# Optimization experiments

Measured on AMD Instinct MI355X. Metric: run time of the kernel, lower is better.

Reference implementation:

```python
import jax, jax.numpy as jnp
import numpy as np

B, L, T = 2048, 512, 32


def setup_inputs() -> dict:
    key = jax.random.key(0)
    k1, k2, k3, k4 = jax.random.split(key, 4)
    emit_score = jax.random.normal(k1, (B, L, T), dtype=jnp.float32)
    transition = jax.random.normal(k2, (T, T), dtype=jnp.float32)
    tags = jax.random.randint(k3, (B, L), 0, T, dtype=jnp.int32)
    lengths = jax.random.randint(k4, (B,), 1, L + 1, dtype=jnp.int32)
    return {"emit_score": emit_score, "transition": transition,
            "tags": tags, "lengths": lengths}


def reference(emit_score, transition, tags, lengths):
    # CRF negative log-likelihood (calculate_loss), per-example loss [B].
    b, l, t = emit_score.shape
    mask = jnp.arange(l)[None, :] < lengths[:, None]          # [B,L] bool
    maskf = mask.astype(emit_score.dtype)

    # --- gold path score ---
    gold = jnp.take_along_axis(emit_score, tags[:, :, None], axis=2)[..., 0]  # [B,L]
    trans_gold = transition[tags[:, :-1], tags[:, 1:]]        # [B,L-1]
    gold = gold.at[:, 1:].add(trans_gold)
    total_score = (gold * maskf).sum(axis=1)                  # [B]

    # --- forward algorithm (log partition) via scan over time ---
    emit_tbT = jnp.transpose(emit_score, (1, 0, 2))           # [L,B,T]
    mask_tb = mask.T                                          # [L,B]

    def step(d, x):
        e_t, m_t = x                                          # [B,T], [B]
        # scores[b, prev, next] = d[b,prev] + transition[prev,next] + e_t[b,next]
        scores = d[:, :, None] + transition[None, :, :] + e_t[:, None, :]
        new_d = jax.nn.logsumexp(scores, axis=1)              # [B,T]
        d = jnp.where(m_t[:, None], new_d, d)                 # freeze finished rows
        return d, None

    d0 = emit_tbT[0]                                          # [B,T]
    d, _ = jax.lax.scan(step, d0, (emit_tbT[1:], mask_tb[1:]))
    log_z = jax.nn.logsumexp(d, axis=1)                       # [B]

    return log_z - total_score                                # loss = -llk
```

## Files before the change

kernel.cpp:

```cpp
#include <hip/hip_runtime.h>


constexpr int TT = 32;
constexpr int LL = 512;

#define L2E  1.4426950408889634f
#define LN2f 0.6931471805599453f

template<int I>
__device__ __forceinline__ float bcastf(float v) {
  return __int_as_float(__builtin_amdgcn_ds_swizzle(__float_as_int(v), (I << 5)));
}
template<int X>
__device__ __forceinline__ float swzxf(float v) {
  return __int_as_float(__builtin_amdgcn_ds_swizzle(__float_as_int(v), (X << 10) | 0x1F));
}
__device__ __forceinline__ float bpermf(int byteaddr, float v) {
  return __int_as_float(__builtin_amdgcn_ds_bpermute(byteaddr, __float_as_int(v)));
}

#define MV4(i0) do { \
    float av0 = bcastf<(i0)>(a);     float av1 = bcastf<(i0)+1>(a); \
    float av2 = bcastf<(i0)+2>(a);   float av3 = bcastf<(i0)+3>(a); \
    acc0 = fmaf(av0, Ec[(i0)],   acc0); acc1 = fmaf(av1, Ec[(i0)+1], acc1); \
    acc2 = fmaf(av2, Ec[(i0)+2], acc2); acc3 = fmaf(av3, Ec[(i0)+3], acc3); \
  } while (0)

__global__ __launch_bounds__(256, 1) void crf_fwd(
    const float* __restrict__ emit, const float* __restrict__ trans,
    const int* __restrict__ tags, const int* __restrict__ lengths,
    float* __restrict__ out, int B)
{
  __shared__ float s_trans[TT * TT];
  {
    const float4* t4 = (const float4*)trans;
    ((float4*)s_trans)[threadIdx.x] = t4[threadIdx.x];
  }
  __syncthreads();

  const int lane = threadIdx.x & 31;
  const int b = blockIdx.x * (blockDim.x >> 5) + (threadIdx.x >> 5);
  if (b >= B) return;
  const int gbase4 = (threadIdx.x & 32) << 2;

  float Ec[TT];
#pragma unroll
  for (int i = 0; i < TT; ++i)
    Ec[i] = __builtin_amdgcn_exp2f(s_trans[i * TT + lane] * L2E);

  const int len = lengths[b];
  const float* erow = emit + (size_t)b * (LL * TT);
  const int*  trow = tags + (size_t)b * LL;

  float e0  = erow[lane];
  int  ptag = trow[0];
  float g   = bpermf((ptag << 2) + gbase4, e0);
  float a   = __builtin_amdgcn_exp2f(e0 * L2E);
  float LS  = 0.f;

  int mlen = max(len, __shfl_xor(len, 32));
  mlen = __builtin_amdgcn_readfirstlane(mlen);
  const int nch = (mlen - 1 + 3) >> 2;

  float eb[4], en[4];
  int   tg[4], tgn[4];
#pragma unroll
  for (int k = 0; k < 4; ++k) {
    int t = 1 + k; int tc = t < LL ? t : LL - 1;
    eb[k] = erow[tc * TT + lane];
    tg[k] = trow[tc];
  }
#pragma unroll
  for (int k = 0; k < 4; ++k) {
    int t = 5 + k; int tc = t < LL ? t : LL - 1;
    en[k] = erow[tc * TT + lane];
    tgn[k] = trow[tc];
  }

  for (int c = 0; c < nch; ++c) {
    const int tb = 1 + (c << 2);

    float ep[4]; int tgp[4];
#pragma unroll
    for (int k = 0; k < 4; ++k) {
      int t = tb + 8 + k; int tc = t < LL ? t : LL - 1;
      ep[k]  = erow[tc * TT + lane];
      tgp[k] = trow[tc];
    }

    float e2v[4];
#pragma unroll
    for (int k = 0; k < 4; ++k) e2v[k] = __builtin_amdgcn_exp2f(eb[k] * L2E);

#pragma unroll
    for (int k = 0; k < 4; ++k) {
      const int t = tb + k;
      float acc0 = 0.f, acc1 = 0.f, acc2 = 0.f, acc3 = 0.f;
      MV4(0); MV4(4); MV4(8); MV4(12); MV4(16); MV4(20); MV4(24); MV4(28);
      float anew = ((acc0 + acc1) + (acc2 + acc3)) * e2v[k];
      const bool valid = t < len;
      a = valid ? anew : a;

      int tag  = tg[k];
      float eg = bpermf((tag << 2) + gbase4, eb[k]);
      float tr = s_trans[(ptag << 5) + tag];
      g += valid ? (eg + tr) : 0.f;
      ptag = tag;
    }

    float m = fmaxf(bcastf<0>(a), 1e-30f);
    float r = __builtin_amdgcn_rcpf(m);
    a *= r;
    LS += __builtin_amdgcn_logf(m);

#pragma unroll
    for (int k = 0; k < 4; ++k) {
      eb[k] = en[k]; tg[k] = tgn[k];
      en[k] = ep[k]; tgn[k] = tgp[k];
    }
  }

  float s = a;
  s += swzxf<1>(s); s += swzxf<2>(s); s += swzxf<4>(s);
  s += swzxf<8>(s); s += swzxf<16>(s);
  float logz = (__builtin_amdgcn_logf(s) + LS) * LN2f;
  if (lane == 0) out[b] = logz - g;
}

extern "C" void kernel_launch(void* const* d_in, const int* in_sizes, int n_in,
                              void* d_out, int out_size, void* d_ws, size_t ws_size,
                              hipStream_t stream) {
  const float* emit    = (const float*)d_in[0];
  const float* trans   = (const float*)d_in[1];
  const int*   tags    = (const int*)d_in[2];
  const int*   lengths = (const int*)d_in[3];
  float*       out     = (float*)d_out;
  const int B = in_sizes[3];
  const int groupsPerBlock = 256 / 32;
  const int blocks = (B + groupsPerBlock - 1) / groupsPerBlock;
  hipLaunchKernelGGL(crf_fwd, dim3(blocks), dim3(256), 0, stream,
                     emit, trans, tags, lengths, out, B);
}
```

Measured before the change: 283.1 us.

## Broadcast alpha through LDS float4 reads and shrink blocks to one wave

Replaces the 32 ds_swizzle broadcasts per step with a store of alpha to shared memory followed by eight float4 LDS reads. Blocks go from 256 threads to 64 (one wave, two sequences), giving 1024 blocks instead of 256 so more of the GPU's compute units get work. The gold-score gather via ds_bpermute becomes a per-lane masked accumulation, reduced by swizzle at the end. This adds an LDS write-read round trip on every time step, with no explicit barrier; it relies on the two sequences sharing one wavefront so the 32-lane groups run in lockstep.

```diff
diff --git a/kernel.cpp b/kernel.cpp
--- a/kernel.cpp
+++ b/kernel.cpp
@@ -15,33 +15,29 @@
 __device__ __forceinline__ float swzxf(float v) {
   return __int_as_float(__builtin_amdgcn_ds_swizzle(__float_as_int(v), (X << 10) | 0x1F));
 }
-__device__ __forceinline__ float bpermf(int byteaddr, float v) {
-  return __int_as_float(__builtin_amdgcn_ds_bpermute(byteaddr, __float_as_int(v)));
-}
 
-#define MV4(i0) do { \
-    float av0 = bcastf<(i0)>(a);     float av1 = bcastf<(i0)+1>(a); \
-    float av2 = bcastf<(i0)+2>(a);   float av3 = bcastf<(i0)+3>(a); \
-    acc0 = fmaf(av0, Ec[(i0)],   acc0); acc1 = fmaf(av1, Ec[(i0)+1], acc1); \
-    acc2 = fmaf(av2, Ec[(i0)+2], acc2); acc3 = fmaf(av3, Ec[(i0)+3], acc3); \
-  } while (0)
-
-__global__ __launch_bounds__(256, 1) void crf_fwd(
+__global__ __launch_bounds__(64) void crf_fwd(
     const float* __restrict__ emit, const float* __restrict__ trans,
     const int* __restrict__ tags, const int* __restrict__ lengths,
     float* __restrict__ out, int B)
 {
-  __shared__ float s_trans[TT * TT];
+  __shared__ float  s_trans[TT * TT];
+  __shared__ float4 s_alpha[2][TT / 4];
+
   {
     const float4* t4 = (const float4*)trans;
-    ((float4*)s_trans)[threadIdx.x] = t4[threadIdx.x];
+    float4* st4 = (float4*)s_trans;
+#pragma unroll
+    for (int k = 0; k < 4; ++k)
+      st4[threadIdx.x + 64 * k] = t4[threadIdx.x + 64 * k];
   }
   __syncthreads();
 
   const int lane = threadIdx.x & 31;
-  const int b = blockIdx.x * (blockDim.x >> 5) + (threadIdx.x >> 5);
+  const int grp  = threadIdx.x >> 5;
+  const int b = blockIdx.x * 2 + grp;
   if (b >= B) return;
-  const int gbase4 = (threadIdx.x & 32) << 2;
+  float* sa = (float*)&s_alpha[grp][0];
 
   float Ec[TT];
 #pragma unroll
@@ -50,13 +46,13 @@
 
   const int len = lengths[b];
   const float* erow = emit + (size_t)b * (LL * TT);
-  const int*  trow = tags + (size_t)b * LL;
+  const int*  trow  = tags + (size_t)b * LL;
 
-  float e0  = erow[lane];
-  int  ptag = trow[0];
-  float g   = bpermf((ptag << 2) + gbase4, e0);
-  float a   = __builtin_amdgcn_exp2f(e0 * L2E);
-  float LS  = 0.f;
+  float e0   = erow[lane];
+  int   ptag = trow[0];
+  float a    = __builtin_amdgcn_exp2f(e0 * L2E);
+  float gacc = (lane == ptag) ? e0 : 0.f;
+  float LS   = 0.f;
 
   int mlen = max(len, __shfl_xor(len, 32));
   mlen = __builtin_amdgcn_readfirstlane(mlen);
@@ -95,16 +91,27 @@
 #pragma unroll
     for (int k = 0; k < 4; ++k) {
       const int t = tb + k;
+
+      sa[lane] = a;
+      float4 A[8];
+#pragma unroll
+      for (int q = 0; q < 8; ++q) A[q] = s_alpha[grp][q];
+
       float acc0 = 0.f, acc1 = 0.f, acc2 = 0.f, acc3 = 0.f;
-      MV4(0); MV4(4); MV4(8); MV4(12); MV4(16); MV4(20); MV4(24); MV4(28);
+#pragma unroll
+      for (int q = 0; q < 8; ++q) {
+        acc0 = fmaf(A[q].x, Ec[4 * q + 0], acc0);
+        acc1 = fmaf(A[q].y, Ec[4 * q + 1], acc1);
+        acc2 = fmaf(A[q].z, Ec[4 * q + 2], acc2);
+        acc3 = fmaf(A[q].w, Ec[4 * q + 3], acc3);
+      }
       float anew = ((acc0 + acc1) + (acc2 + acc3)) * e2v[k];
       const bool valid = t < len;
       a = valid ? anew : a;
 
       int tag  = tg[k];
-      float eg = bpermf((tag << 2) + gbase4, eb[k]);
-      float tr = s_trans[(ptag << 5) + tag];
-      g += valid ? (eg + tr) : 0.f;
+      float tr = s_trans[(ptag << 5) + lane];
+      gacc += ((lane == tag) && valid) ? (eb[k] + tr) : 0.f;
       ptag = tag;
     }
 
@@ -120,11 +127,16 @@
     }
   }
 
-  float s = a;
-  s += swzxf<1>(s); s += swzxf<2>(s); s += swzxf<4>(s);
-  s += swzxf<8>(s); s += swzxf<16>(s);
+  float s  = a;
+  float gs = gacc;
+  s += swzxf<1>(s);   gs += swzxf<1>(gs);
+  s += swzxf<2>(s);   gs += swzxf<2>(gs);
+  s += swzxf<4>(s);   gs += swzxf<4>(gs);
+  s += swzxf<8>(s);   gs += swzxf<8>(gs);
+  s += swzxf<16>(s);  gs += swzxf<16>(gs);
+
   float logz = (__builtin_amdgcn_logf(s) + LS) * LN2f;
-  if (lane == 0) out[b] = logz - g;
+  if (lane == 0) out[b] = logz - gs;
 }
 
 extern "C" void kernel_launch(void* const* d_in, const int* in_sizes, int n_in,
@@ -136,8 +148,7 @@
   const int*   lengths = (const int*)d_in[3];
   float*       out     = (float*)d_out;
   const int B = in_sizes[3];
-  const int groupsPerBlock = 256 / 32;
-  const int blocks = (B + groupsPerBlock - 1) / groupsPerBlock;
-  hipLaunchKernelGGL(crf_fwd, dim3(blocks), dim3(256), 0, stream,
+  const int blocks = (B + 1) / 2;
+  hipLaunchKernelGGL(crf_fwd, dim3(blocks), dim3(64), 0, stream,
                      emit, trans, tags, lengths, out, B);
 }
```

After: 273.2 us. 1.04x faster.
